# Kernel tuning notes

Measured on AMD Instinct MI355X. Metric: run time of the kernel, lower is better.

The kernel has to match this reference:

```python
import jax, jax.numpy as jnp
import numpy as np

N_EMBD = 256
N_HEAD = 8
HEAD_DIM = N_EMBD            # per-head dim == n_embd in this module
N_QKV = N_EMBD * N_HEAD      # 2048
B, T = 4, 2048
NEG = -1e30


def _rope(x, cos, sin):
    # x: [B, T+1, H, D]; cos/sin: [T+1, 1, D//2]
    d = x.shape[-1] // 2
    x1, x2 = x[..., :d], x[..., d:]
    y1 = x1 * cos + x2 * sin
    y2 = -x1 * sin + x2 * cos
    return jnp.concatenate([y1, y2], axis=-1)


def _rmsnorm(x):
    eps = jnp.finfo(x.dtype).eps
    return x * jax.lax.rsqrt(jnp.mean(x * x, axis=-1, keepdims=True) + eps)


def setup_inputs() -> dict:
    key = jax.random.key(0)
    k0, k1, k2, k3 = jax.random.split(key, 4)
    x = jax.random.normal(k0, (B, T, N_EMBD), jnp.float32)
    # rotary tables for T+1 positions (sink token at position 0)
    d = HEAD_DIM // 2
    pos = jnp.arange(T + 1, dtype=jnp.float32)[:, None]
    inv_freq = 1.0 / (10000.0 ** (jnp.arange(d, dtype=jnp.float32) / d))
    ang = pos * inv_freq[None, :]
    cos = jnp.cos(ang)[:, None, :]  # [T+1, 1, d]
    sin = jnp.sin(ang)[:, None, :]
    W_qkvg = jax.random.normal(k1, (4 * N_QKV, N_EMBD), jnp.float32) * 0.02
    W_sink = jax.random.normal(k2, (1, N_EMBD), jnp.float32) * 0.02
    W_out = jax.random.normal(k3, (N_EMBD, N_QKV), jnp.float32) * 0.02
    tao = jnp.array([1.2, 1.2], jnp.float32)
    return {"x": x, "cos": cos, "sin": sin, "W_qkvg": W_qkvg,
            "W_sink": W_sink, "W_out": W_out, "tao": tao, "n_head": N_HEAD}


def reference(x, cos, sin, W_qkvg, W_sink, W_out, tao, n_head):
    Bv, Tv, C = x.shape
    # prepend learned sink token
    s = jnp.broadcast_to(W_sink[None, :, :], (Bv, 1, C))
    x0 = jnp.concatenate([s, x], axis=1)                     # [B, T+1, C]
    qkvg = (x0 @ W_qkvg.T).reshape(Bv, Tv + 1, n_head, -1)   # [B, T+1, H, 4*hd]
    q, k, v, g = jnp.split(qkvg, 4, axis=-1)                 # each [B, T+1, H, hd]
    q = _rmsnorm(_rope(q, cos, sin)) * tao[0]
    k = _rmsnorm(_rope(k, cos, sin)) * tao[1]
    q, k, v, g = (a.transpose(0, 2, 1, 3) for a in (q, k, v, g))  # [B, H, T+1, hd]
    hd = q.shape[-1]
    scores = jnp.einsum("bhqd,bhkd->bhqk", q, k) / jnp.sqrt(jnp.asarray(hd, q.dtype))
    mask = jnp.tril(jnp.ones((Tv + 1, Tv + 1), bool))
    scores = jnp.where(mask, scores, NEG)
    p = jax.nn.softmax(scores, axis=-1)
    y = jnp.einsum("bhqk,bhkd->bhqd", p, v) * jax.nn.sigmoid(g)
    y = y.transpose(0, 2, 1, 3).reshape(Bv, Tv + 1, -1)[:, 1:, :]  # drop sink
    return y @ W_out.T
```

## Files before the change

kernel.cpp:

```cpp
#include <hip/hip_runtime.h>
#include <stdint.h>

#define DEVI __device__ __forceinline__

typedef __attribute__((ext_vector_type(8))) short bf16x8;
typedef __attribute__((ext_vector_type(4))) float f32x4;
typedef __attribute__((ext_vector_type(4))) unsigned short u16x4;
typedef unsigned short u16;
typedef unsigned int u32;

#define TT 2049
#define BH 32
#define MPAD 8320
#define MREAL 8196
#define NQ 8192
#define KDIM 256
#define VTP 2112

#define SBAR() __builtin_amdgcn_s_barrier()
#define MEMFENCE() asm volatile("" ::: "memory")
#define VMCNT(n) asm volatile("s_waitcnt vmcnt(" #n ")" ::: "memory")
#define LGKMCNT0() asm volatile("s_waitcnt lgkmcnt(0)" ::: "memory")

DEVI u16 f2bf(float f) {
    union { float f; u32 u; } v; v.f = f;
    u32 r = v.u + 0x7FFF + ((v.u >> 16) & 1);
    return (u16)(r >> 16);
}
DEVI float bf2f(u16 h) {
    union { u32 u; float f; } v; v.u = ((u32)h) << 16;
    return v.f;
}

#define GLD16(src, lds) __builtin_amdgcn_global_load_lds( \
    (const __attribute__((address_space(1))) void*)(src), \
    (__attribute__((address_space(3))) void*)(lds), 16, 0, 0)

#define CN0 (MPAD * 64)
#define CN1 (NQ * 64)
#define CN2 (256 * 512)
__global__ void k_conv_all(const float* __restrict__ x, const float* __restrict__ wsink,
                           const float* __restrict__ wqkvg, const float* __restrict__ wout,
                           u16* __restrict__ x0b, u16* __restrict__ wqb, u16* __restrict__ wob) {
    int idx = blockIdx.x * 256 + threadIdx.x;
    const float* src = nullptr;
    u16* dst = nullptr;
    int oidx = idx;
    bool zero_fill = false;
    if (idx < CN0) {
        int m = idx >> 6, c = (idx & 63) << 2;
        if (m < MREAL) {
            int b = m / TT, t = m - b * TT;
            src = (t == 0) ? (wsink + c) : (x + ((size_t)((b << 11) + t - 1) << 8) + c);
        } else zero_fill = true;
        dst = x0b;
    } else if (idx < CN0 + CN1) {
        oidx = idx - CN0;
        src = wqkvg + ((size_t)oidx << 2);
        dst = wqb;
    } else if (idx < CN0 + CN1 + CN2) {
        oidx = idx - CN0 - CN1;
        src = wout + ((size_t)oidx << 2);
        dst = wob;
    } else return;
    f32x4 v = {0.f, 0.f, 0.f, 0.f};
    if (!zero_fill) v = *(const f32x4*)src;
    union { u16 h[4]; uint2 u2; } o;
#pragma unroll
    for (int i = 0; i < 4; ++i) o.h[i] = f2bf(v[i]);
    *(uint2*)(dst + ((size_t)oidx << 2)) = o.u2;
}

__global__ __launch_bounds__(512) void k_gemm_qkvg(const u16* __restrict__ A, const u16* __restrict__ Bm,
                                                   const float* __restrict__ cosb, const float* __restrict__ sinb,
                                                   const float* __restrict__ tao,
                                                   u16* __restrict__ Qb, u16* __restrict__ Kb,
                                                   u16* __restrict__ Vt, u16* __restrict__ Gb) {
    __shared__ __align__(16) u16 ldsW[256 * 64];
    __shared__ __align__(16) u16 ldsX[128 * 64];
    __shared__ float rowsum[128 * 4];
    const int tid = threadIdx.x, l = tid & 63, w = tid >> 6;
    const int row0 = blockIdx.x * 128;
    const int gcol0 = blockIdx.y * 256;
    const int h = gcol0 >> 10, ty = (gcol0 & 1023) >> 8;
    const int g = w >> 1, thalf = w & 1;
    f32x4 acc[4][4];
    const f32x4 zero = {0.f, 0.f, 0.f, 0.f};
#pragma unroll
    for (int i = 0; i < 4; ++i)
#pragma unroll
        for (int j = 0; j < 4; ++j) acc[i][j] = zero;

    for (int kt = 0; kt < KDIM; kt += 64) {
        __syncthreads();
#pragma unroll
        for (int it = 0; it < 4; ++it) {
            int lin = (it * 512 + tid) * 16;
            int r = lin >> 7, cb = lin & 127;
            int scb = cb ^ ((r & 7) << 4);
            GLD16((const char*)(Bm + (size_t)(gcol0 + r) * KDIM + kt) + scb,
                  (char*)ldsW + it * 8192 + w * 1024);
        }
#pragma unroll
        for (int it = 0; it < 2; ++it) {
            int lin = (it * 512 + tid) * 16;
            int r = lin >> 7, cb = lin & 127;
            int scb = cb ^ ((r & 7) << 4);
            GLD16((const char*)(A + (size_t)(row0 + r) * KDIM + kt) + scb,
                  (char*)ldsX + it * 8192 + w * 1024);
        }
        __syncthreads();
#pragma unroll
        for (int kk = 0; kk < 64; kk += 32) {
            bf16x8 af[4], bfr[4];
            int cbyte = (kk + ((l >> 4) << 3)) * 2;
#pragma unroll
            for (int mi = 0; mi < 4; ++mi) {
                int rr = g * 32 + (mi & 1) * 16 + (mi >> 1) * 128 + (l & 15);
                af[mi] = *(const bf16x8*)((const char*)ldsW + ((rr * 128 + cbyte) ^ ((rr & 7) << 4)));
            }
#pragma unroll
            for (int ni = 0; ni < 4; ++ni) {
                int rr = thalf * 64 + ni * 16 + (l & 15);
                bfr[ni] = *(const bf16x8*)((const char*)ldsX + ((rr * 128 + cbyte) ^ ((rr & 7) << 4)));
            }
#pragma unroll
            for (int mi = 0; mi < 4; ++mi)
#pragma unroll
                for (int ni = 0; ni < 4; ++ni)
                    acc[mi][ni] = __builtin_amdgcn_mfma_f32_16x16x32_bf16(af[mi], bfr[ni], acc[mi][ni], 0, 0, 0);
        }
    }
    const float eps = 1.1920928955078125e-07f;
    if (ty < 2) {
#pragma unroll
        for (int ni = 0; ni < 4; ++ni) {
            float ss = 0.f;
#pragma unroll
            for (int mi = 0; mi < 4; ++mi)
#pragma unroll
                for (int r = 0; r < 4; ++r) { float v = acc[mi][ni][r]; ss += v * v; }
            ss += __shfl_xor(ss, 16, 64);
            ss += __shfl_xor(ss, 32, 64);
            if (l < 16) {
                int trow = thalf * 64 + ni * 16 + l;
                rowsum[trow * 4 + g] = ss;
            }
        }
        __syncthreads();
        const float tv = (ty == 0) ? tao[0] * 0.0625f : tao[1];
        u16* Obuf = (ty == 0) ? Qb : Kb;
#pragma unroll
        for (int ni = 0; ni < 4; ++ni) {
            int trow = thalf * 64 + ni * 16 + (l & 15);
            int grow = row0 + trow;
            if (grow >= MREAL) continue;
            int b = grow / TT, t = grow - b * TT;
            f32x4 rsv = *(const f32x4*)(rowsum + trow * 4);
            float rs = rsv[0] + rsv[1] + rsv[2] + rsv[3];
            float scale = rsqrtf(rs * (1.0f / 256.0f) + eps) * tv;
            u16* dst = Obuf + ((size_t)((b * 8 + h) * TT + t) << 8);
#pragma unroll
            for (int mih = 0; mih < 2; ++mih) {
                int d0 = g * 32 + mih * 16 + ((l >> 4) << 2);
                f32x4 cv = *(const f32x4*)(cosb + t * 128 + d0);
                f32x4 sv = *(const f32x4*)(sinb + t * 128 + d0);
                u16x4 lo, hi;
#pragma unroll
                for (int r = 0; r < 4; ++r) {
                    float xlo = acc[mih][ni][r], xhi = acc[mih + 2][ni][r];
                    lo[r] = f2bf((xlo * cv[r] + xhi * sv[r]) * scale);
                    hi[r] = f2bf((xhi * cv[r] - xlo * sv[r]) * scale);
                }
                *(u16x4*)(dst + d0) = lo;
                *(u16x4*)(dst + d0 + 128) = hi;
            }
        }
    } else {
#pragma unroll
        for (int ni = 0; ni < 4; ++ni) {
            int trow = thalf * 64 + ni * 16 + (l & 15);
            int grow = row0 + trow;
            if (grow >= MREAL) continue;
            int b = grow / TT, t = grow - b * TT;
            int bh = b * 8 + h;
            if (ty == 3) {
                u16* dst = Gb + ((size_t)(bh * TT + t) << 8);
#pragma unroll
                for (int mi = 0; mi < 4; ++mi) {
                    int d0 = g * 32 + (mi & 1) * 16 + (mi >> 1) * 128 + ((l >> 4) << 2);
                    u16x4 pk;
#pragma unroll
                    for (int r = 0; r < 4; ++r) pk[r] = f2bf(acc[mi][ni][r]);
                    *(u16x4*)(dst + d0) = pk;
                }
            } else {
#pragma unroll
                for (int mi = 0; mi < 4; ++mi) {
                    int d0 = g * 32 + (mi & 1) * 16 + (mi >> 1) * 128 + ((l >> 4) << 2);
#pragma unroll
                    for (int r = 0; r < 4; ++r)
                        Vt[(size_t)(bh * 256 + d0 + r) * VTP + t] = f2bf(acc[mi][ni][r]);
                }
            }
        }
    }
}

__global__ __launch_bounds__(512) void k_attn(const u16* __restrict__ Qb, const u16* __restrict__ Kb,
                                              const u16* __restrict__ Vt, const u16* __restrict__ Gb,
                                              const float* __restrict__ tao,
                                              u16* __restrict__ Y) {
    __shared__ __align__(16) u16 Kt[2][64 * 256];
    __shared__ __align__(16) u16 Vl[2][256 * 64];
    __shared__ __align__(16) u16 Plds[8][16 * 64];
    const int tid = threadIdx.x, l = tid & 63, w = tid >> 6;
    const int qt = 15 - (blockIdx.x >> 5);
    const int bh = blockIdx.x & 31;
    const int b = bh >> 3, h = bh & 7;
    const int g0 = (w >> 1) * 2;
    const int kvh = (w & 1) * 32;
    const int dh = (w & 1) * 128;
    const int mq_g0 = qt * 128 + g0 * 16 + 1;
    const size_t qkbase = (size_t)bh * TT * 256;
    const size_t vrow0 = (size_t)bh * 256;
    const float Cs = tao[0] * tao[1] * 16.0f;

    bf16x8 aq[2][8];
#pragma unroll
    for (int g = 0; g < 2; ++g) {
        int mq = mq_g0 + g * 16 + (l & 15);
        const u16* qp = Qb + qkbase + ((size_t)mq << 8) + ((l >> 4) << 3);
#pragma unroll
        for (int kk = 0; kk < 8; ++kk) aq[g][kk] = *(const bf16x8*)(qp + kk * 32);
    }
    bf16x8 vone;
#pragma unroll
    for (int i = 0; i < 8; ++i) vone[i] = (short)0x3F80;
    f32x4 acc[2][8], accs[2];
    const f32x4 zero = {0.f, 0.f, 0.f, 0.f};
#pragma unroll
    for (int g = 0; g < 2; ++g) {
#pragma unroll
        for (int i = 0; i < 8; ++i) acc[g][i] = zero;
        accs[g] = zero;
    }

    const int nkv = 2 * qt + 3;

    auto STAGE = [&](int j, int bufi) {
        const int kv0 = j << 6;
#pragma unroll
        for (int it = 0; it < 4; ++it) {
            int lin = (it * 512 + tid) * 16;
            {
                int r = lin >> 9, cbyt = lin & 511;
                int scb = cbyt ^ ((r & 7) << 4);
                int krow = kv0 + r; if (krow > 2048) krow = 2048;
                GLD16((const char*)(Kb + qkbase + ((size_t)krow << 8)) + scb,
                      (char*)&Kt[bufi][0] + it * 8192 + w * 1024);
            }
            {
                int vr = lin >> 7, cb = lin & 127;
                int scb = cb ^ ((vr & 7) << 4);
                GLD16((const char*)(Vt + (vrow0 + vr) * VTP + kv0) + scb,
                      (char*)&Vl[bufi][0] + it * 8192 + w * 1024);
            }
        }
    };

    STAGE(0, 0);
    int buf = 0;

    for (int j = 0; j < nkv; ++j) {
        const int kv0 = j << 6;
        if (j + 1 < nkv) { STAGE(j + 1, buf ^ 1); VMCNT(8); }
        else             { VMCNT(0); }
        SBAR(); MEMFENCE();

        const bool active = (kv0 <= mq_g0 + 31);
        if (active) {
            f32x4 s[2][2];
#pragma unroll
            for (int g = 0; g < 2; ++g) { s[g][0] = zero; s[g][1] = zero; }
            __builtin_amdgcn_s_setprio(1);
#pragma unroll
            for (int kk = 0; kk < 8; ++kk) {
                int cbyte = kk * 64 + ((l >> 4) << 4);
#pragma unroll
                for (int t = 0; t < 2; ++t) {
                    int rr = kvh + t * 16 + (l & 15);
                    bf16x8 bk = *(const bf16x8*)((const char*)&Kt[buf][0] + ((rr * 512 + cbyte) ^ ((rr & 7) << 4)));
#pragma unroll
                    for (int g = 0; g < 2; ++g)
                        s[g][t] = __builtin_amdgcn_mfma_f32_16x16x32_bf16(aq[g][kk], bk, s[g][t], 0, 0, 0);
                }
            }
            __builtin_amdgcn_s_setprio(0);
#pragma unroll
            for (int g = 0; g < 2; ++g) {
                char* pwb = (char*)&Plds[g0 + g][0];
                const bool needmask = (kv0 + kvh + 31 > mq_g0 + g * 16);
#pragma unroll
                for (int t = 0; t < 2; ++t)
#pragma unroll
                    for (int r = 0; r < 4; ++r) {
                        float sv = s[g][t][r];
                        if (needmask) {
                            int kg = kv0 + kvh + t * 16 + (l & 15);
                            int qg = mq_g0 + g * 16 + ((l >> 4) << 2) + r;
                            if (kg > qg) sv = -1e30f;
                        }
                        float pv = __expf(sv - Cs);
                        int row = ((l >> 4) << 2) + r;
                        int byte = row * 128 + (kvh + t * 16 + (l & 15)) * 2;
                        *(u16*)(pwb + (byte ^ ((row & 7) << 4))) = f2bf(pv);
                    }
            }
        }
        LGKMCNT0(); SBAR(); MEMFENCE();

        if (active) {
            bf16x8 ap[2][2];
#pragma unroll
            for (int g = 0; g < 2; ++g) {
                const char* prb = (const char*)&Plds[g0 + g][0];
                int row = l & 15;
                int b0 = row * 128 + ((l >> 4) << 4);
                ap[g][0] = *(const bf16x8*)(prb + (b0 ^ ((row & 7) << 4)));
                ap[g][1] = *(const bf16x8*)(prb + ((b0 + 64) ^ ((row & 7) << 4)));
            }
            __builtin_amdgcn_s_setprio(1);
#pragma unroll
            for (int df = 0; df < 8; ++df) {
                int vr = dh + df * 16 + (l & 15);
                int cbase = vr * 128 + ((l >> 4) << 4);
                bf16x8 bv0 = *(const bf16x8*)((const char*)&Vl[buf][0] + (cbase ^ ((vr & 7) << 4)));
                bf16x8 bv1 = *(const bf16x8*)((const char*)&Vl[buf][0] + ((cbase + 64) ^ ((vr & 7) << 4)));
#pragma unroll
                for (int g = 0; g < 2; ++g) {
                    acc[g][df] = __builtin_amdgcn_mfma_f32_16x16x32_bf16(ap[g][0], bv0, acc[g][df], 0, 0, 0);
                    acc[g][df] = __builtin_amdgcn_mfma_f32_16x16x32_bf16(ap[g][1], bv1, acc[g][df], 0, 0, 0);
                }
            }
#pragma unroll
            for (int g = 0; g < 2; ++g) {
                accs[g] = __builtin_amdgcn_mfma_f32_16x16x32_bf16(ap[g][0], vone, accs[g], 0, 0, 0);
                accs[g] = __builtin_amdgcn_mfma_f32_16x16x32_bf16(ap[g][1], vone, accs[g], 0, 0, 0);
            }
            __builtin_amdgcn_s_setprio(0);
        }
        MEMFENCE(); SBAR();
        buf ^= 1;
    }
#pragma unroll
    for (int g = 0; g < 2; ++g)
#pragma unroll
        for (int r = 0; r < 4; ++r) {
            int mq = mq_g0 + g * 16 + ((l >> 4) << 2) + r;
            float inv = 1.0f / accs[g][r];
            const u16* gp = Gb + qkbase + ((size_t)mq << 8) + dh + (l & 15);
            u16* yp = Y + ((size_t)(b * 2048 + mq - 1)) * 2048 + h * 256 + dh + (l & 15);
#pragma unroll
            for (int df = 0; df < 8; ++df) {
                float g2 = bf2f(gp[df * 16]);
                float sg = 1.0f / (1.0f + __expf(-g2));
                yp[df * 16] = f2bf(acc[g][df][r] * inv * sg);
            }
        }
}

__global__ __launch_bounds__(256) void k_gemm_out(const u16* __restrict__ A, const u16* __restrict__ Bm,
                                                  float* __restrict__ Cout) {
    __shared__ __align__(16) u16 ldsA[64 * 64];
    __shared__ __align__(16) u16 ldsB[64 * 64];
    const int tid = threadIdx.x;
    const int l = tid & 63, w = tid >> 6;
    const int row0 = blockIdx.x * 64, col0 = blockIdx.y * 64;
    const int mbase = (w >> 1) * 32, nbase = (w & 1) * 32;
    const int K2 = 2048;
    f32x4 acc[2][2];
    const f32x4 zero = {0.f, 0.f, 0.f, 0.f};
#pragma unroll
    for (int i = 0; i < 2; ++i)
#pragma unroll
        for (int j = 0; j < 2; ++j) acc[i][j] = zero;

    for (int kt = 0; kt < K2; kt += 64) {
        __syncthreads();
#pragma unroll
        for (int it = 0; it < 2; ++it) {
            int lin = (it * 256 + tid) * 16;
            int r = lin >> 7;
            int cb = lin & 127;
            int scb = cb ^ ((r & 7) << 4);
            GLD16((const char*)(A + (size_t)(row0 + r) * K2 + kt) + scb,
                  (char*)ldsA + it * 4096 + w * 1024);
            GLD16((const char*)(Bm + (size_t)(col0 + r) * K2 + kt) + scb,
                  (char*)ldsB + it * 4096 + w * 1024);
        }
        __syncthreads();
#pragma unroll
        for (int kk = 0; kk < 64; kk += 32) {
            bf16x8 af[2], bfr[2];
            int cbyte = (kk + ((l >> 4) << 3)) * 2;
#pragma unroll
            for (int mi = 0; mi < 2; ++mi) {
                int rr = mbase + mi * 16 + (l & 15);
                af[mi] = *(const bf16x8*)((const char*)ldsA + ((rr * 128 + cbyte) ^ ((rr & 7) << 4)));
            }
#pragma unroll
            for (int ni = 0; ni < 2; ++ni) {
                int rr = nbase + ni * 16 + (l & 15);
                bfr[ni] = *(const bf16x8*)((const char*)ldsB + ((rr * 128 + cbyte) ^ ((rr & 7) << 4)));
            }
#pragma unroll
            for (int mi = 0; mi < 2; ++mi)
#pragma unroll
                for (int ni = 0; ni < 2; ++ni)
                    acc[mi][ni] = __builtin_amdgcn_mfma_f32_16x16x32_bf16(af[mi], bfr[ni], acc[mi][ni], 0, 0, 0);
        }
    }
#pragma unroll
    for (int mi = 0; mi < 2; ++mi)
#pragma unroll
        for (int ni = 0; ni < 2; ++ni)
#pragma unroll
            for (int r = 0; r < 4; ++r) {
                int grow = row0 + mbase + mi * 16 + ((l >> 4) << 2) + r;
                int gcol = col0 + nbase + ni * 16 + (l & 15);
                Cout[(size_t)grow * 256 + gcol] = acc[mi][ni][r];
            }
}

extern "C" void kernel_launch(void* const* d_in, const int* in_sizes, int n_in,
                              void* d_out, int out_size, void* d_ws, size_t ws_size,
                              hipStream_t stream) {
    const float* x     = (const float*)d_in[0];
    const float* cosb  = (const float*)d_in[1];
    const float* sinb  = (const float*)d_in[2];
    const float* wqkvg = (const float*)d_in[3];
    const float* wsink = (const float*)d_in[4];
    const float* wout  = (const float*)d_in[5];
    const float* tao   = (const float*)d_in[6];
    float* out = (float*)d_out;

    char* ws = (char*)d_ws;
    u16* x0b = (u16*)(ws + 0);
    u16* wqb = (u16*)(ws + 4259840);
    u16* wob = (u16*)(ws + 8454144);
    u16* Qb  = (u16*)(ws + 9502720);
    u16* Kb  = (u16*)(ws + 43073536);
    u16* Gb  = (u16*)(ws + 76644352);
    u16* Vt  = (u16*)(ws + 110215168);
    u16* Yb  = (u16*)(ws + 144818176);

    k_conv_all<<<dim3((CN0 + CN1 + CN2 + 255) / 256), 256, 0, stream>>>(
        x, wsink, wqkvg, wout, x0b, wqb, wob);
    k_gemm_qkvg<<<dim3(65, 32), 512, 0, stream>>>(x0b, wqb, cosb, sinb, tao, Qb, Kb, Vt, Gb);
    k_attn<<<dim3(16 * 32), 512, 0, stream>>>(Qb, Kb, Vt, Gb, tao, Yb);
    k_gemm_out<<<dim3(128, 4), 256, 0, stream>>>(Yb, wob, out);
}
```

Measured before the change: 227.1 us.

## Stage QKVG projection epilogue through LDS for coalesced global stores

The projection kernel's epilogue now writes its bf16 results into a swizzled LDS tile, reusing the weight buffer, and then drains full rows with 16-byte coalesced stores for Q, K and G. For the transposed V output, lanes now write consecutive t positions instead of scattered 2-byte strided stores. The goal is to cut the number of uncoalesced global write transactions. The cost is extra LDS traffic and several block-wide barriers in the epilogue.

```diff
diff --git a/kernel.cpp b/kernel.cpp
--- a/kernel.cpp
+++ b/kernel.cpp
@@ -132,6 +132,22 @@
         }
     }
     const float eps = 1.1920928955078125e-07f;
+    char* Ct = (char*)ldsW;
+
+    auto DRAIN_ROWS = [&](u16* gbase, int dH) {
+#pragma unroll
+        for (int p = 0; p < 4; ++p) {
+            int t = p * 32 + (tid >> 4);
+            int grow = row0 + t;
+            if (grow < MREAL) {
+                int b = grow / TT, tt = grow - b * TT;
+                int byte = (t * 256 + (tid & 15) * 16) ^ ((t & 7) << 4);
+                bf16x8 v = *(const bf16x8*)(Ct + byte);
+                *(bf16x8*)(gbase + (((size_t)((b * 8 + h) * TT + tt)) << 8) + dH + (tid & 15) * 8) = v;
+            }
+        }
+    };
+
     if (ty < 2) {
 #pragma unroll
         for (int ni = 0; ni < 4; ++ni) {
@@ -150,59 +166,109 @@
         __syncthreads();
         const float tv = (ty == 0) ? tao[0] * 0.0625f : tao[1];
         u16* Obuf = (ty == 0) ? Qb : Kb;
+        u16x4 lov[4][2], hiv[4][2];
 #pragma unroll
         for (int ni = 0; ni < 4; ++ni) {
             int trow = thalf * 64 + ni * 16 + (l & 15);
             int grow = row0 + trow;
-            if (grow >= MREAL) continue;
             int b = grow / TT, t = grow - b * TT;
+            if (grow >= MREAL) { b = 0; t = 0; }
             f32x4 rsv = *(const f32x4*)(rowsum + trow * 4);
             float rs = rsv[0] + rsv[1] + rsv[2] + rsv[3];
             float scale = rsqrtf(rs * (1.0f / 256.0f) + eps) * tv;
-            u16* dst = Obuf + ((size_t)((b * 8 + h) * TT + t) << 8);
 #pragma unroll
             for (int mih = 0; mih < 2; ++mih) {
                 int d0 = g * 32 + mih * 16 + ((l >> 4) << 2);
                 f32x4 cv = *(const f32x4*)(cosb + t * 128 + d0);
                 f32x4 sv = *(const f32x4*)(sinb + t * 128 + d0);
-                u16x4 lo, hi;
 #pragma unroll
                 for (int r = 0; r < 4; ++r) {
                     float xlo = acc[mih][ni][r], xhi = acc[mih + 2][ni][r];
-                    lo[r] = f2bf((xlo * cv[r] + xhi * sv[r]) * scale);
-                    hi[r] = f2bf((xhi * cv[r] - xlo * sv[r]) * scale);
+                    lov[ni][mih][r] = f2bf((xlo * cv[r] + xhi * sv[r]) * scale);
+                    hiv[ni][mih][r] = f2bf((xhi * cv[r] - xlo * sv[r]) * scale);
                 }
-                *(u16x4*)(dst + d0) = lo;
-                *(u16x4*)(dst + d0 + 128) = hi;
-            }
+            }
+        }
+#pragma unroll
+        for (int ni = 0; ni < 4; ++ni)
+#pragma unroll
+            for (int mih = 0; mih < 2; ++mih) {
+                int t = thalf * 64 + ni * 16 + (l & 15);
+                int dd = g * 32 + mih * 16 + ((l >> 4) << 2);
+                int byte = (t * 256 + dd * 2) ^ ((t & 7) << 4);
+                *(u16x4*)(Ct + byte) = lov[ni][mih];
+            }
+        __syncthreads();
+        DRAIN_ROWS(Obuf, 0);
+        __syncthreads();
+#pragma unroll
+        for (int ni = 0; ni < 4; ++ni)
+#pragma unroll
+            for (int mih = 0; mih < 2; ++mih) {
+                int t = thalf * 64 + ni * 16 + (l & 15);
+                int dd = g * 32 + mih * 16 + ((l >> 4) << 2);
+                int byte = (t * 256 + dd * 2) ^ ((t & 7) << 4);
+                *(u16x4*)(Ct + byte) = hiv[ni][mih];
+            }
+        __syncthreads();
+        DRAIN_ROWS(Obuf, 128);
+    } else if (ty == 3) {
+        __syncthreads();
+#pragma unroll
+        for (int half = 0; half < 2; ++half) {
+#pragma unroll
+            for (int mi2 = 0; mi2 < 2; ++mi2) {
+                int mi = half * 2 + mi2;
+#pragma unroll
+                for (int ni = 0; ni < 4; ++ni) {
+                    int t = thalf * 64 + ni * 16 + (l & 15);
+                    int dd = g * 32 + (mi & 1) * 16 + ((l >> 4) << 2);
+                    u16x4 pk;
+#pragma unroll
+                    for (int r = 0; r < 4; ++r) pk[r] = f2bf(acc[mi][ni][r]);
+                    int byte = (t * 256 + dd * 2) ^ ((t & 7) << 4);
+                    *(u16x4*)(Ct + byte) = pk;
+                }
+            }
+            __syncthreads();
+            DRAIN_ROWS(Gb, half * 128);
+            if (half == 0) __syncthreads();
         }
     } else {
-#pragma unroll
-        for (int ni = 0; ni < 4; ++ni) {
-            int trow = thalf * 64 + ni * 16 + (l & 15);
-            int grow = row0 + trow;
-            if (grow >= MREAL) continue;
-            int b = grow / TT, t = grow - b * TT;
-            int bh = b * 8 + h;
-            if (ty == 3) {
-                u16* dst = Gb + ((size_t)(bh * TT + t) << 8);
-#pragma unroll
-                for (int mi = 0; mi < 4; ++mi) {
-                    int d0 = g * 32 + (mi & 1) * 16 + (mi >> 1) * 128 + ((l >> 4) << 2);
-                    u16x4 pk;
-#pragma unroll
-                    for (int r = 0; r < 4; ++r) pk[r] = f2bf(acc[mi][ni][r]);
-                    *(u16x4*)(dst + d0) = pk;
+        __syncthreads();
+        int grow0 = row0 + l, grow1 = row0 + l + 64;
+        int b0_ = grow0 / TT, t0_ = grow0 - b0_ * TT;
+        int b1_ = grow1 / TT, t1_ = grow1 - b1_ * TT;
+        bool v0 = grow0 < MREAL, v1 = grow1 < MREAL;
+#pragma unroll
+        for (int half = 0; half < 2; ++half) {
+#pragma unroll
+            for (int mi2 = 0; mi2 < 2; ++mi2) {
+                int mi = half * 2 + mi2;
+#pragma unroll
+                for (int ni = 0; ni < 4; ++ni) {
+                    int t = thalf * 64 + ni * 16 + (l & 15);
+#pragma unroll
+                    for (int r = 0; r < 4; ++r) {
+                        int dd = g * 32 + (mi & 1) * 16 + ((l >> 4) << 2) + r;
+                        int byte = (dd * 256 + t * 2) ^ (((dd >> 2) & 7) << 4);
+                        *(u16*)(Ct + byte) = f2bf(acc[mi][ni][r]);
+                    }
                 }
-            } else {
-#pragma unroll
-                for (int mi = 0; mi < 4; ++mi) {
-                    int d0 = g * 32 + (mi & 1) * 16 + (mi >> 1) * 128 + ((l >> 4) << 2);
-#pragma unroll
-                    for (int r = 0; r < 4; ++r)
-                        Vt[(size_t)(bh * 256 + d0 + r) * VTP + t] = f2bf(acc[mi][ni][r]);
-                }
-            }
+            }
+            __syncthreads();
+#pragma unroll
+            for (int p = 0; p < 16; ++p) {
+                int dloc = p * 8 + w;
+                int d = half * 128 + dloc;
+                int byte0 = (dloc * 256 + l * 2) ^ (((dloc >> 2) & 7) << 4);
+                int byte1 = (dloc * 256 + (l + 64) * 2) ^ (((dloc >> 2) & 7) << 4);
+                u16 q0 = *(const u16*)(Ct + byte0);
+                u16 q1 = *(const u16*)(Ct + byte1);
+                if (v0) Vt[((size_t)((b0_ * 8 + h) * 256 + d)) * VTP + t0_] = q0;
+                if (v1) Vt[((size_t)((b1_ * 8 + h) * 256 + d)) * VTP + t1_] = q1;
+            }
+            if (half == 0) __syncthreads();
         }
     }
 }
```

Result: slower. 231.7 us (+2.0%).
